# Optimization experiments

Hardware: AMD Instinct MI355X
Metric: run time of the kernel (lower is better)

## Reference

```python
import jax, jax.numpy as jnp
import numpy as np

NUM_HEADS = 12
D_T, D_H, D_W = 192, 288, 288  # rope_dims for embed_dim=768


def rotate_half(x):
    x1, x2 = jnp.split(x, 2, axis=-1)
    return jnp.concatenate([-x2, x1], axis=-1)


def apply_rope(qk, cos_t, sin_t, cos_h, sin_h, cos_w, sin_w, t_idx, h_idx, w_idx):
    # qk: (B, N, C); rotate the three dim-chunks with per-token gathered tables
    qk_t = qk[..., :D_T]
    qk_h = qk[..., D_T:D_T + D_H]
    qk_w = qk[..., D_T + D_H:]
    qk_t = qk_t * cos_t[t_idx] + rotate_half(qk_t) * sin_t[t_idx]
    qk_h = qk_h * cos_h[h_idx] + rotate_half(qk_h) * sin_h[h_idx]
    qk_w = qk_w * cos_w[w_idx] + rotate_half(qk_w) * sin_w[w_idx]
    return jnp.concatenate([qk_t, qk_h, qk_w], axis=-1)


def setup_inputs() -> dict:
    key = jax.random.key(0)
    ks = jax.random.split(key, 12)
    B, N, C = 2, 2048, 768
    T, Hs, Ws = 8, 16, 16  # N = T*Hs*Ws
    x = jax.random.normal(ks[0], (B, N, C), dtype=jnp.float32)
    Wqkv = jax.random.normal(ks[1], (C, 3 * C), dtype=jnp.float32) * (C ** -0.5)
    Wout = jax.random.normal(ks[2], (C, C), dtype=jnp.float32) * (C ** -0.5)
    cos_t = jax.random.uniform(ks[3], (T, D_T), dtype=jnp.float32)
    sin_t = jax.random.uniform(ks[4], (T, D_T), dtype=jnp.float32)
    cos_h = jax.random.uniform(ks[5], (Hs, D_H), dtype=jnp.float32)
    sin_h = jax.random.uniform(ks[6], (Hs, D_H), dtype=jnp.float32)
    cos_w = jax.random.uniform(ks[7], (Ws, D_W), dtype=jnp.float32)
    sin_w = jax.random.uniform(ks[8], (Ws, D_W), dtype=jnp.float32)
    t_idx = jax.random.randint(ks[9], (N,), 0, T, dtype=jnp.int32)
    h_idx = jax.random.randint(ks[10], (N,), 0, Hs, dtype=jnp.int32)
    w_idx = jax.random.randint(ks[11], (N,), 0, Ws, dtype=jnp.int32)
    return {"x": x, "Wqkv": Wqkv, "Wout": Wout,
            "cos_t": cos_t, "sin_t": sin_t, "cos_h": cos_h, "sin_h": sin_h,
            "cos_w": cos_w, "sin_w": sin_w,
            "t_idx": t_idx, "h_idx": h_idx, "w_idx": w_idx}


def reference(x, Wqkv, Wout, cos_t, sin_t, cos_h, sin_h, cos_w, sin_w, t_idx, h_idx, w_idx):
    B, N, C = x.shape
    Hd = C // NUM_HEADS
    scale = Hd ** -0.5
    qkv = (x @ Wqkv).reshape(B, N, 3, C)
    q, k, v = qkv[:, :, 0], qkv[:, :, 1], qkv[:, :, 2]
    # RoPE applied to full embedding dim BEFORE head split
    q = apply_rope(q, cos_t, sin_t, cos_h, sin_h, cos_w, sin_w, t_idx, h_idx, w_idx)
    k = apply_rope(k, cos_t, sin_t, cos_h, sin_h, cos_w, sin_w, t_idx, h_idx, w_idx)
    q = q.reshape(B, N, NUM_HEADS, Hd).transpose(0, 2, 1, 3)
    k = k.reshape(B, N, NUM_HEADS, Hd).transpose(0, 2, 1, 3)
    v = v.reshape(B, N, NUM_HEADS, Hd).transpose(0, 2, 1, 3)
    attn = jnp.einsum('bhqd,bhkd->bhqk', q, k) * scale
    attn = jax.nn.softmax(attn, axis=-1)
    out = jnp.einsum('bhqk,bhkd->bhqd', attn, v)
    out = out.transpose(0, 2, 1, 3).reshape(B, N, C)
    return out @ Wout
```

## Files before the change

kernel.cpp:

```cpp
#include <hip/hip_runtime.h>
#include <hip/hip_bf16.h>
#include <math.h>

#define BB 2
#define NN 2048
#define CC 768
#define NHEAD 12
#define HD 64
#define C3 2304
#define NSP 2

typedef __attribute__((ext_vector_type(8))) _Float16 half8;
typedef __attribute__((ext_vector_type(8))) short short8;
typedef __attribute__((ext_vector_type(4))) float f32x4;
typedef __attribute__((ext_vector_type(4))) unsigned uint4v;
#define MFMAH(a, b, c) \
  __builtin_amdgcn_mfma_f32_16x16x32_f16(a, b, c, 0, 0, 0)

__device__ __forceinline__ float fast_exp2(float x) {
  return __builtin_amdgcn_exp2f(x);
}
__device__ __forceinline__ ushort f2h(float x) {
  _Float16 h = (_Float16)x;
  return __builtin_bit_cast(ushort, h);
}
__device__ __forceinline__ float h2f(ushort u) {
  return (float)__builtin_bit_cast(_Float16, u);
}
__device__ __forceinline__ unsigned pk2h(float a, float b) {
  return __builtin_bit_cast(unsigned, __builtin_amdgcn_cvt_pkrtz(a, b));
}
__device__ __forceinline__ void gload_lds16(const void* gsrc, void* lds) {
  __builtin_amdgcn_global_load_lds(
      (const __attribute__((address_space(1))) unsigned int*)gsrc,
      (__attribute__((address_space(3))) unsigned int*)lds, 16, 0, 0);
}
__device__ __forceinline__ half8 ld_h8(const ushort* p) {
  return __builtin_bit_cast(half8, *reinterpret_cast<const short8*>(p));
}

__global__ __launch_bounds__(256) void conv_rows_kernel(const float* __restrict__ X,
                                                        ushort* __restrict__ Xf) {
  int idx = blockIdx.x * 256 + threadIdx.x;
  const float4 v0 = *reinterpret_cast<const float4*>(&X[(size_t)idx * 8]);
  const float4 v1 = *reinterpret_cast<const float4*>(&X[(size_t)idx * 8 + 4]);
  ushort h[8] = {f2h(v0.x), f2h(v0.y), f2h(v0.z), f2h(v0.w),
                 f2h(v1.x), f2h(v1.y), f2h(v1.z), f2h(v1.w)};
  *reinterpret_cast<uint4*>(&Xf[(size_t)idx * 8]) = *reinterpret_cast<uint4*>(h);
}

__global__ __launch_bounds__(256) void conv_transpose_kernel(const float* __restrict__ W,
                                                             ushort* __restrict__ Wf,
                                                             int N) {
  __shared__ float t[32][33];
  const int tx = threadIdx.x & 31, ty = threadIdx.x >> 5;
  const int n0 = blockIdx.x * 32, k0 = blockIdx.y * 32;
#pragma unroll
  for (int r = 0; r < 4; r++) {
    int kk = ty + r * 8;
    t[kk][tx] = W[(size_t)(k0 + kk) * N + n0 + tx];
  }
  __syncthreads();
#pragma unroll
  for (int r = 0; r < 4; r++) {
    int nn = ty + r * 8;
    Wf[(size_t)(n0 + nn) * CC + k0 + tx] = f2h(t[tx][nn]);
  }
}

template <int BM, bool F16OUT>
__global__ __launch_bounds__(256) void gemm_f16_kernel(const ushort* __restrict__ A,
                                                       const ushort* __restrict__ B,
                                                       void* __restrict__ Cout, int Nn) {
  constexpr int WM = BM / 2;
  constexpr int MR = WM / 16;
  constexpr int NR = 3;
  __shared__ __align__(16) ushort Asm[BM * 64];
  __shared__ __align__(16) ushort Bsm[96 * 64];
  const int tid = threadIdx.x;
  const int lane = tid & 63, w = tid >> 6;
  const int l15 = lane & 15, lg = lane >> 4;
  const int wr = w >> 1, wc = w & 1;
  const int m0 = blockIdx.y * BM, n0 = blockIdx.x * 96;
  const int srow = lane >> 3, lc = lane & 7;
  const int scp = lc ^ (srow & 7);

  f32x4 acc[MR][NR];
#pragma unroll
  for (int m = 0; m < MR; m++)
#pragma unroll
    for (int n = 0; n < NR; n++) acc[m][n] = (f32x4){0.f, 0.f, 0.f, 0.f};

  for (int k0 = 0; k0 < 768; k0 += 64) {
#pragma unroll
    for (int it = 0; it < BM / 32; it++) {
      int r0 = it * 32 + w * 8;
      int row = r0 + srow;
      gload_lds16(A + (size_t)(m0 + row) * CC + k0 + scp * 8, &Asm[r0 * 64]);
    }
#pragma unroll
    for (int it = 0; it < 3; it++) {
      int r0 = it * 32 + w * 8;
      int row = r0 + srow;
      gload_lds16(B + (size_t)(n0 + row) * CC + k0 + scp * 8, &Bsm[r0 * 64]);
    }
    __syncthreads();

    half8 ah[MR][2], bh[NR][2];
#pragma unroll
    for (int m = 0; m < MR; m++) {
      int row = wr * WM + m * 16 + l15;
#pragma unroll
      for (int s = 0; s < 2; s++)
        ah[m][s] = ld_h8(&Asm[row * 64 + ((s * 4 + lg) ^ (row & 7)) * 8]);
    }
#pragma unroll
    for (int n = 0; n < NR; n++) {
      int col = wc * 48 + n * 16 + l15;
#pragma unroll
      for (int s = 0; s < 2; s++)
        bh[n][s] = ld_h8(&Bsm[col * 64 + ((s * 4 + lg) ^ (col & 7)) * 8]);
    }
#pragma unroll
    for (int s = 0; s < 2; s++)
#pragma unroll
      for (int m = 0; m < MR; m++)
#pragma unroll
        for (int n = 0; n < NR; n++)
          acc[m][n] = MFMAH(ah[m][s], bh[n][s], acc[m][n]);
    __syncthreads();
  }

#pragma unroll
  for (int m = 0; m < MR; m++)
#pragma unroll
    for (int j = 0; j < 4; j++) {
      int row = m0 + wr * WM + m * 16 + lg * 4 + j;
#pragma unroll
      for (int n = 0; n < NR; n++) {
        int col = n0 + wc * 48 + n * 16 + l15;
        if constexpr (F16OUT) {
          ((ushort*)Cout)[(size_t)row * Nn + col] = f2h(acc[m][n][j]);
        } else {
          ((float*)Cout)[(size_t)row * Nn + col] = acc[m][n][j];
        }
      }
    }
}

__global__ __launch_bounds__(256) void rope_f16_kernel(
    const ushort* __restrict__ qkvh, const float* __restrict__ cos_t,
    const float* __restrict__ sin_t, const float* __restrict__ cos_h,
    const float* __restrict__ sin_h, const float* __restrict__ cos_w,
    const float* __restrict__ sin_w, const int* __restrict__ t_idx,
    const int* __restrict__ h_idx, const int* __restrict__ w_idx,
    ushort* __restrict__ Qf, ushort* __restrict__ Kf) {
  const int tok = blockIdx.x;
  const int b = tok >> 11, n = tok & 2047;
  const int ti = t_idx[n], hi = h_idx[n], wi = w_idx[n];
  const ushort* base = qkvh + (size_t)tok * C3;
  const float QSC = 0.125f * 1.44269504088896f;

#pragma unroll
  for (int s = 0; s < 3; s++) {
    int j = threadIdx.x + s * 256;
    float c, sn, sign;
    int pj;
    if (j < 192) {
      int jj = j;
      c = cos_t[ti * 192 + jj];
      sn = sin_t[ti * 192 + jj];
      pj = (jj < 96) ? j + 96 : j - 96;
      sign = (jj < 96) ? -1.f : 1.f;
    } else if (j < 480) {
      int jj = j - 192;
      c = cos_h[hi * 288 + jj];
      sn = sin_h[hi * 288 + jj];
      pj = (jj < 144) ? j + 144 : j - 144;
      sign = (jj < 144) ? -1.f : 1.f;
    } else {
      int jj = j - 480;
      c = cos_w[wi * 288 + jj];
      sn = sin_w[wi * 288 + jj];
      pj = (jj < 144) ? j + 144 : j - 144;
      sign = (jj < 144) ? -1.f : 1.f;
    }
    float qv = h2f(base[j]), kv = h2f(base[768 + j]);
    float qp = h2f(base[pj]) * sign, kp = h2f(base[768 + pj]) * sign;
    float qr = fmaf(qv, c, qp * sn) * QSC;
    float kr = fmaf(kv, c, kp * sn);
    int h = j >> 6, d = j & 63;
    int bh = b * NHEAD + h;
    size_t o = ((size_t)bh * NN + n) * HD + d;
    Qf[o] = f2h(qr);
    Kf[o] = f2h(kr);
  }
}

__global__ __launch_bounds__(256) void v_transpose_kernel(const ushort* __restrict__ qkvh,
                                                          ushort* __restrict__ Vt) {
  __shared__ ushort t[64][70];
  const int bh = blockIdx.y;
  const int n0 = blockIdx.x * 64;
  const int b = bh / NHEAD, h = bh % NHEAD;
  const int row = threadIdx.x >> 2;
  const int c0 = (threadIdx.x & 3) * 16;
  const ushort* src = qkvh + (size_t)(b * NN + n0 + row) * C3 + 1536 + h * 64 + c0;
  ushort tmp16[16];
  *reinterpret_cast<uint4*>(tmp16) = *reinterpret_cast<const uint4*>(src);
  *reinterpret_cast<uint4*>(tmp16 + 8) = *reinterpret_cast<const uint4*>(src + 8);
#pragma unroll
  for (int i = 0; i < 16; i++) t[row][c0 + i] = tmp16[i];
  __syncthreads();
  const int d = threadIdx.x >> 2;
  const int tk0 = (threadIdx.x & 3) * 16;
  ushort tmp[16];
#pragma unroll
  for (int i = 0; i < 16; i++) tmp[i] = t[tk0 + i][d];
  ushort* dst = Vt + ((size_t)bh * HD + d) * NN + n0 + tk0;
  *reinterpret_cast<uint4*>(dst) = *reinterpret_cast<uint4*>(tmp);
  *reinterpret_cast<uint4*>(dst + 8) = *reinterpret_cast<uint4*>(tmp + 8);
}

__global__ __launch_bounds__(256, 6) void attn_mfma_kernel(
    const ushort* __restrict__ Qf, const ushort* __restrict__ Kf,
    const ushort* __restrict__ Vt, float* __restrict__ PartO,
    float* __restrict__ Partml) {
  __shared__ __align__(16) ushort smemK[4096];
  __shared__ __align__(16) ushort smemV[2][4096];
  const int tid = threadIdx.x;
  const int lane = tid & 63, w = tid >> 6;
  const int l15 = lane & 15, lg = lane >> 4;
  const int qt = blockIdx.x;
  const int bh = blockIdx.y;
  const int sp = blockIdx.z;
  const size_t kbase = (size_t)bh * NN * HD;
  const size_t vbase = (size_t)bh * HD * NN;

  half8 qf[2];
  {
    const int r = qt * 64 + w * 16 + l15;
#pragma unroll
    for (int s = 0; s < 2; s++)
      qf[s] = ld_h8(Qf + kbase + (size_t)r * HD + s * 32 + lg * 8);
  }

  const int srow = lane >> 3;
  const int sc = (lane & 7) ^ srow;

#define STAGE_K(kt_)                                                           \
  {                                                                            \
    _Pragma("unroll") for (int it = 0; it < 2; it++) {                         \
      int r0 = it * 32 + w * 8;                                                \
      int r = r0 + srow;                                                       \
      gload_lds16(Kf + kbase + (size_t)((kt_)*64 + r) * 64 + sc * 8,           \
                  &smemK[r0 * 64]);                                            \
    }                                                                          \
  }
#define STAGE_V(kt_, vb_)                                                      \
  {                                                                            \
    _Pragma("unroll") for (int it = 0; it < 2; it++) {                         \
      int r0 = it * 32 + w * 8;                                                \
      int r = r0 + srow;                                                       \
      gload_lds16(Vt + vbase + (size_t)r * NN + (kt_)*64 + sc * 8,             \
                  &smemV[vb_][r0 * 64]);                                       \
    }                                                                          \
  }

  f32x4 o_acc[4];
#pragma unroll
  for (int g = 0; g < 4; g++) o_acc[g] = (f32x4){0.f, 0.f, 0.f, 0.f};
  float m_run = -INFINITY, l_run = 0.f;

  const int rmask7 = l15 & 7;
  const int gsel0 = (lg < 2) ? 0 : 1;
  const bool send_own = ((lg ^ (lg >> 1)) & 1) != 0;
  const int kt0 = sp * (32 / NSP), ktend = kt0 + (32 / NSP);

  STAGE_V(kt0, 0);
  STAGE_K(kt0);

  for (int kt = kt0; kt < ktend; kt++) {
    const int cur = (kt - kt0) & 1;
    __syncthreads();
    if (kt + 1 < ktend) STAGE_V(kt + 1, cur ^ 1);

    f32x4 s_acc[4];
#pragma unroll
    for (int g = 0; g < 4; g++) s_acc[g] = (f32x4){0.f, 0.f, 0.f, 0.f};
    __builtin_amdgcn_s_setprio(1);
#pragma unroll
    for (int g = 0; g < 4; g++) {
      const int r = g * 16 + l15;
#pragma unroll
      for (int s = 0; s < 2; s++) {
        half8 ka = ld_h8(&smemK[r * 64 + ((s * 4 + lg) ^ rmask7) * 8]);
        s_acc[g] = MFMAH(ka, qf[s], s_acc[g]);
      }
    }
    __builtin_amdgcn_s_setprio(0);

    __syncthreads();
    if (kt + 1 < ktend) STAGE_K(kt + 1);

    float m0a = fmaxf(fmaxf(s_acc[0][0], s_acc[0][1]), fmaxf(s_acc[0][2], s_acc[0][3]));
    float m1a = fmaxf(fmaxf(s_acc[1][0], s_acc[1][1]), fmaxf(s_acc[1][2], s_acc[1][3]));
    float m2a = fmaxf(fmaxf(s_acc[2][0], s_acc[2][1]), fmaxf(s_acc[2][2], s_acc[2][3]));
    float m3a = fmaxf(fmaxf(s_acc[3][0], s_acc[3][1]), fmaxf(s_acc[3][2], s_acc[3][3]));
    float pm = fmaxf(fmaxf(m0a, m1a), fmaxf(m2a, m3a));
    pm = fmaxf(pm, __shfl_xor(pm, 16, 64));
    pm = fmaxf(pm, __shfl_xor(pm, 32, 64));
    if (!__all(pm - m_run <= 8.0f)) {
      const float mn = fmaxf(m_run, pm);
      const float corr = fast_exp2(m_run - mn);
      m_run = mn;
      l_run *= corr;
#pragma unroll
      for (int g = 0; g < 4; g++)
#pragma unroll
        for (int j = 0; j < 4; j++) o_acc[g][j] *= corr;
    }
    float p[4][4];
#pragma unroll
    for (int g = 0; g < 4; g++)
#pragma unroll
      for (int j = 0; j < 4; j++) {
        p[g][j] = fast_exp2(s_acc[g][j] - m_run);
        l_run += p[g][j];
      }

    unsigned w0[4], w1[4];
#pragma unroll
    for (int g = 0; g < 4; g++) {
      w0[g] = pk2h(p[g][0], p[g][1]);
      w1[g] = pk2h(p[g][2], p[g][3]);
    }
    const int c0 = gsel0 ^ 1, c1 = c0 + 2;
    unsigned o0 = w0[gsel0], o1 = w1[gsel0], o2 = w0[gsel0 + 2], o3 = w1[gsel0 + 2];
    unsigned r0v = __shfl_xor((int)w0[c0], 32, 64);
    unsigned r1v = __shfl_xor((int)w1[c0], 32, 64);
    unsigned r2v = __shfl_xor((int)w0[c1], 32, 64);
    unsigned r3v = __shfl_xor((int)w1[c1], 32, 64);
    unsigned p0 = send_own ? o0 : r0v, p1 = send_own ? o1 : r1v;
    unsigned p2 = send_own ? o2 : r2v, p3 = send_own ? o3 : r3v;
    unsigned k0v = send_own ? r0v : o0, k1v = send_own ? r1v : o1;
    unsigned k2v = send_own ? r2v : o2, k3v = send_own ? r3v : o3;
    unsigned n0 = __shfl_xor((int)p0, 16, 64);
    unsigned n1 = __shfl_xor((int)p1, 16, 64);
    unsigned n2 = __shfl_xor((int)p2, 16, 64);
    unsigned n3 = __shfl_xor((int)p3, 16, 64);
    const bool lgeven = (lg & 1) == 0;
    uint4v bv0 = lgeven ? (uint4v){k0v, k1v, n0, n1} : (uint4v){n0, n1, k0v, k1v};
    uint4v bv1 = lgeven ? (uint4v){k2v, k3v, n2, n3} : (uint4v){n2, n3, k2v, k3v};
    half8 pb[2] = {__builtin_bit_cast(half8, bv0), __builtin_bit_cast(half8, bv1)};

    __builtin_amdgcn_s_setprio(1);
#pragma unroll
    for (int kk = 0; kk < 2; kk++)
#pragma unroll
      for (int g = 0; g < 4; g++) {
        half8 va =
            ld_h8(&smemV[cur][(g * 16 + l15) * 64 + ((kk * 4 + lg) ^ rmask7) * 8]);
        o_acc[g] = MFMAH(va, pb[kk], o_acc[g]);
      }
    __builtin_amdgcn_s_setprio(0);
  }

  l_run += __shfl_xor(l_run, 16, 64);
  l_run += __shfl_xor(l_run, 32, 64);
  const int q = qt * 64 + w * 16 + l15;
  const size_t pidx = ((size_t)(sp * 24 + bh) * NN + q);
#pragma unroll
  for (int g = 0; g < 4; g++) {
    *reinterpret_cast<float4*>(&PartO[pidx * 64 + g * 16 + lg * 4]) =
        make_float4(o_acc[g][0], o_acc[g][1], o_acc[g][2], o_acc[g][3]);
  }
  if (lg == 0) {
    Partml[pidx * 2] = m_run;
    Partml[pidx * 2 + 1] = l_run;
  }
#undef STAGE_K
#undef STAGE_V
}

__global__ __launch_bounds__(256) void attn_combine_kernel(
    const float* __restrict__ PartO, const float* __restrict__ Partml,
    ushort* __restrict__ Attnf) {
  const int qt = blockIdx.x;
  const int bh = blockIdx.y;
  const int b = bh / NHEAD, h = bh % NHEAD;
  const int tid = threadIdx.x;
  const int q = qt * 64 + (tid >> 2);
  const int d0 = (tid & 3) * 16;

  size_t idx[NSP];
  float mv[NSP], lv[NSP];
  float m = -INFINITY;
#pragma unroll
  for (int s = 0; s < NSP; s++) {
    idx[s] = ((size_t)(s * 24 + bh) * NN + q);
    mv[s] = Partml[idx[s] * 2];
    lv[s] = Partml[idx[s] * 2 + 1];
    m = fmaxf(m, mv[s]);
  }
  float wsum = 0.f, wgt[NSP];
#pragma unroll
  for (int s = 0; s < NSP; s++) {
    wgt[s] = fast_exp2(mv[s] - m);
    wsum += lv[s] * wgt[s];
  }
  const float inv = 1.0f / wsum;

  ushort hv[16];
#pragma unroll
  for (int d = 0; d < 16; d += 4) {
    float acc[4] = {0.f, 0.f, 0.f, 0.f};
#pragma unroll
    for (int s = 0; s < NSP; s++) {
      float4 a = *reinterpret_cast<const float4*>(&PartO[idx[s] * 64 + d0 + d]);
      acc[0] = fmaf(a.x, wgt[s], acc[0]);
      acc[1] = fmaf(a.y, wgt[s], acc[1]);
      acc[2] = fmaf(a.z, wgt[s], acc[2]);
      acc[3] = fmaf(a.w, wgt[s], acc[3]);
    }
#pragma unroll
    for (int i = 0; i < 4; i++) hv[d + i] = f2h(acc[i] * inv);
  }
  ushort* dst = Attnf + (size_t)(b * NN + q) * CC + h * 64 + d0;
  *reinterpret_cast<uint4*>(dst) = *reinterpret_cast<uint4*>(hv);
  *reinterpret_cast<uint4*>(dst + 8) = *reinterpret_cast<uint4*>(hv + 8);
}

extern "C" void kernel_launch(void* const* d_in, const int* in_sizes, int n_in,
                              void* d_out, int out_size, void* d_ws, size_t ws_size,
                              hipStream_t stream) {
  const float* x = (const float*)d_in[0];
  const float* Wqkv = (const float*)d_in[1];
  const float* Wout = (const float*)d_in[2];
  const float* cos_t = (const float*)d_in[3];
  const float* sin_t = (const float*)d_in[4];
  const float* cos_h = (const float*)d_in[5];
  const float* sin_h = (const float*)d_in[6];
  const float* cos_w = (const float*)d_in[7];
  const float* sin_w = (const float*)d_in[8];
  const int* t_idx = (const int*)d_in[9];
  const int* h_idx = (const int*)d_in[10];
  const int* w_idx = (const int*)d_in[11];
  float* out = (float*)d_out;

  const size_t R0 = (size_t)4096 * 2304;
  float* ws = (float*)d_ws;
  ushort* qkvh = (ushort*)ws;
  float* PartO = ws;
  ushort* us = (ushort*)(ws + R0);
  const size_t HS = (size_t)24 * 2048 * 64;
  ushort* Qf = us;
  ushort* Kf = Qf + HS;
  ushort* Vt = Kf + HS;
  ushort* xf = Vt + HS;
  ushort* wqf = xf + (size_t)4096 * 768;
  ushort* wof = wqf + (size_t)2304 * 768;
  ushort* attnf = wof + (size_t)768 * 768;
  float* Partml = (float*)(attnf + (size_t)4096 * 768);

  conv_rows_kernel<<<dim3(4096 * 768 / 8 / 256), 256, 0, stream>>>(x, xf);
  conv_transpose_kernel<<<dim3(C3 / 32, CC / 32), 256, 0, stream>>>(Wqkv, wqf, C3);
  conv_transpose_kernel<<<dim3(CC / 32, CC / 32), 256, 0, stream>>>(Wout, wof, CC);
  gemm_f16_kernel<128, true><<<dim3(C3 / 96, 4096 / 128), 256, 0, stream>>>(xf, wqf,
                                                                            qkvh, C3);
  rope_f16_kernel<<<dim3(BB * NN), 256, 0, stream>>>(qkvh, cos_t, sin_t, cos_h, sin_h,
                                                     cos_w, sin_w, t_idx, h_idx, w_idx,
                                                     Qf, Kf);
  v_transpose_kernel<<<dim3(NN / 64, BB * NHEAD), 256, 0, stream>>>(qkvh, Vt);
  attn_mfma_kernel<<<dim3(NN / 64, BB * NHEAD, NSP), 256, 0, stream>>>(Qf, Kf, Vt,
                                                                       PartO, Partml);
  attn_combine_kernel<<<dim3(NN / 64, BB * NHEAD), 256, 0, stream>>>(PartO, Partml,
                                                                     attnf);
  gemm_f16_kernel<64, false><<<dim3(CC / 96, 4096 / 64), 256, 0, stream>>>(attnf, wof,
                                                                           out, CC);
}
```

Before: 118.0 us.

## Drop split-K attention and fuse normalization into attention kernel epilogue

Removes the two-way key split of the attention kernel and its separate combine kernel. Each block now iterates over all key tiles and writes normalized fp16 output directly to the attention buffer. This saves a kernel launch and the fp32 partial-output round trip through memory. In exchange the grid shrinks to 768 blocks with twice the serial work each, which lowers parallelism across the GPU's compute units. The workspace layout is also compacted because the partial buffers are gone.

```diff
diff --git a/kernel.cpp b/kernel.cpp
--- a/kernel.cpp
+++ b/kernel.cpp
@@ -8,7 +8,6 @@
 #define NHEAD 12
 #define HD 64
 #define C3 2304
-#define NSP 2
 
 typedef __attribute__((ext_vector_type(8))) _Float16 half8;
 typedef __attribute__((ext_vector_type(8))) short short8;
@@ -224,8 +223,7 @@
 
 __global__ __launch_bounds__(256, 6) void attn_mfma_kernel(
     const ushort* __restrict__ Qf, const ushort* __restrict__ Kf,
-    const ushort* __restrict__ Vt, float* __restrict__ PartO,
-    float* __restrict__ Partml) {
+    const ushort* __restrict__ Vt, ushort* __restrict__ Attnf) {
   __shared__ __align__(16) ushort smemK[4096];
   __shared__ __align__(16) ushort smemV[2][4096];
   const int tid = threadIdx.x;
@@ -233,7 +231,7 @@
   const int l15 = lane & 15, lg = lane >> 4;
   const int qt = blockIdx.x;
   const int bh = blockIdx.y;
-  const int sp = blockIdx.z;
+  const int b = bh / NHEAD, h = bh % NHEAD;
   const size_t kbase = (size_t)bh * NN * HD;
   const size_t vbase = (size_t)bh * HD * NN;
 
@@ -275,15 +273,14 @@
   const int rmask7 = l15 & 7;
   const int gsel0 = (lg < 2) ? 0 : 1;
   const bool send_own = ((lg ^ (lg >> 1)) & 1) != 0;
-  const int kt0 = sp * (32 / NSP), ktend = kt0 + (32 / NSP);
-
-  STAGE_V(kt0, 0);
-  STAGE_K(kt0);
-
-  for (int kt = kt0; kt < ktend; kt++) {
-    const int cur = (kt - kt0) & 1;
+
+  STAGE_V(0, 0);
+  STAGE_K(0);
+
+  for (int kt = 0; kt < NN / 64; kt++) {
+    const int cur = kt & 1;
     __syncthreads();
-    if (kt + 1 < ktend) STAGE_V(kt + 1, cur ^ 1);
+    if (kt + 1 < NN / 64) STAGE_V(kt + 1, cur ^ 1);
 
     f32x4 s_acc[4];
 #pragma unroll
@@ -301,7 +298,7 @@
     __builtin_amdgcn_s_setprio(0);
 
     __syncthreads();
-    if (kt + 1 < ktend) STAGE_K(kt + 1);
+    if (kt + 1 < NN / 64) STAGE_K(kt + 1);
 
     float m0a = fmaxf(fmaxf(s_acc[0][0], s_acc[0][1]), fmaxf(s_acc[0][2], s_acc[0][3]));
     float m1a = fmaxf(fmaxf(s_acc[1][0], s_acc[1][1]), fmaxf(s_acc[1][2], s_acc[1][3]));
@@ -368,67 +365,17 @@
 
   l_run += __shfl_xor(l_run, 16, 64);
   l_run += __shfl_xor(l_run, 32, 64);
+  const float inv = 1.0f / l_run;
   const int q = qt * 64 + w * 16 + l15;
-  const size_t pidx = ((size_t)(sp * 24 + bh) * NN + q);
+  ushort* dst = Attnf + (size_t)(b * NN + q) * CC + h * 64;
 #pragma unroll
   for (int g = 0; g < 4; g++) {
-    *reinterpret_cast<float4*>(&PartO[pidx * 64 + g * 16 + lg * 4]) =
-        make_float4(o_acc[g][0], o_acc[g][1], o_acc[g][2], o_acc[g][3]);
-  }
-  if (lg == 0) {
-    Partml[pidx * 2] = m_run;
-    Partml[pidx * 2 + 1] = l_run;
+    unsigned lo = pk2h(o_acc[g][0] * inv, o_acc[g][1] * inv);
+    unsigned hi = pk2h(o_acc[g][2] * inv, o_acc[g][3] * inv);
+    *reinterpret_cast<uint2*>(dst + g * 16 + lg * 4) = make_uint2(lo, hi);
   }
 #undef STAGE_K
 #undef STAGE_V
-}
-
-__global__ __launch_bounds__(256) void attn_combine_kernel(
-    const float* __restrict__ PartO, const float* __restrict__ Partml,
-    ushort* __restrict__ Attnf) {
-  const int qt = blockIdx.x;
-  const int bh = blockIdx.y;
-  const int b = bh / NHEAD, h = bh % NHEAD;
-  const int tid = threadIdx.x;
-  const int q = qt * 64 + (tid >> 2);
-  const int d0 = (tid & 3) * 16;
-
-  size_t idx[NSP];
-  float mv[NSP], lv[NSP];
-  float m = -INFINITY;
-#pragma unroll
-  for (int s = 0; s < NSP; s++) {
-    idx[s] = ((size_t)(s * 24 + bh) * NN + q);
-    mv[s] = Partml[idx[s] * 2];
-    lv[s] = Partml[idx[s] * 2 + 1];
-    m = fmaxf(m, mv[s]);
-  }
-  float wsum = 0.f, wgt[NSP];
-#pragma unroll
-  for (int s = 0; s < NSP; s++) {
-    wgt[s] = fast_exp2(mv[s] - m);
-    wsum += lv[s] * wgt[s];
-  }
-  const float inv = 1.0f / wsum;
-
-  ushort hv[16];
-#pragma unroll
-  for (int d = 0; d < 16; d += 4) {
-    float acc[4] = {0.f, 0.f, 0.f, 0.f};
-#pragma unroll
-    for (int s = 0; s < NSP; s++) {
-      float4 a = *reinterpret_cast<const float4*>(&PartO[idx[s] * 64 + d0 + d]);
-      acc[0] = fmaf(a.x, wgt[s], acc[0]);
-      acc[1] = fmaf(a.y, wgt[s], acc[1]);
-      acc[2] = fmaf(a.z, wgt[s], acc[2]);
-      acc[3] = fmaf(a.w, wgt[s], acc[3]);
-    }
-#pragma unroll
-    for (int i = 0; i < 4; i++) hv[d + i] = f2h(acc[i] * inv);
-  }
-  ushort* dst = Attnf + (size_t)(b * NN + q) * CC + h * 64 + d0;
-  *reinterpret_cast<uint4*>(dst) = *reinterpret_cast<uint4*>(hv);
-  *reinterpret_cast<uint4*>(dst + 8) = *reinterpret_cast<uint4*>(hv + 8);
 }
 
 extern "C" void kernel_launch(void* const* d_in, const int* in_sizes, int n_in,
@@ -448,11 +395,9 @@
   const int* w_idx = (const int*)d_in[11];
   float* out = (float*)d_out;
 
-  const size_t R0 = (size_t)4096 * 2304;
   float* ws = (float*)d_ws;
   ushort* qkvh = (ushort*)ws;
-  float* PartO = ws;
-  ushort* us = (ushort*)(ws + R0);
+  ushort* us = (ushort*)(ws + (size_t)4096 * 2304 / 2);
   const size_t HS = (size_t)24 * 2048 * 64;
   ushort* Qf = us;
   ushort* Kf = Qf + HS;
@@ -461,7 +406,6 @@
   ushort* wqf = xf + (size_t)4096 * 768;
   ushort* wof = wqf + (size_t)2304 * 768;
   ushort* attnf = wof + (size_t)768 * 768;
-  float* Partml = (float*)(attnf + (size_t)4096 * 768);
 
   conv_rows_kernel<<<dim3(4096 * 768 / 8 / 256), 256, 0, stream>>>(x, xf);
   conv_transpose_kernel<<<dim3(C3 / 32, CC / 32), 256, 0, stream>>>(Wqkv, wqf, C3);
@@ -472,10 +416,7 @@
                                                      cos_w, sin_w, t_idx, h_idx, w_idx,
                                                      Qf, Kf);
   v_transpose_kernel<<<dim3(NN / 64, BB * NHEAD), 256, 0, stream>>>(qkvh, Vt);
-  attn_mfma_kernel<<<dim3(NN / 64, BB * NHEAD, NSP), 256, 0, stream>>>(Qf, Kf, Vt,
-                                                                       PartO, Partml);
-  attn_combine_kernel<<<dim3(NN / 64, BB * NHEAD), 256, 0, stream>>>(PartO, Partml,
-                                                                     attnf);
+  attn_mfma_kernel<<<dim3(NN / 64, BB * NHEAD), 256, 0, stream>>>(Qf, Kf, Vt, attnf);
   gemm_f16_kernel<64, false><<<dim3(CC / 96, 4096 / 64), 256, 0, stream>>>(attnf, wof,
                                                                            out, CC);
 }
```

Result: no change. 118.9 us (+0.8%).
